# Kernel optimization log

Hardware: AMD Instinct MI355X
Metric: run time of the kernel (lower is better)

The kernel has to match this reference:

```python
import jax, jax.numpy as jnp
import numpy as np

MAX_SPAN_LEN = 6

def setup_inputs() -> dict:
    key = jax.random.key(0)
    k1, k2 = jax.random.split(key)
    B, L, H = 16, 1024, 768
    span_adjacency = jax.random.uniform(k1, (B, L, L, 1), dtype=jnp.float32)
    bound_hidden = jax.random.normal(k2, (B, L, H), dtype=jnp.float32)
    return {"span_adjacency": span_adjacency, "bound_hidden": bound_hidden}

def reference(span_adjacency, bound_hidden):
    # out[:, j] = sum_{i=j}^{min(j+6,L)-1} w[:,j,i] * concat(h[:,i], h[:,j])
    B, L, H = bound_hidden.shape
    d = jnp.arange(MAX_SPAN_LEN)                      # window offsets [6]
    j = jnp.arange(L)                                  # [L]
    idx = jnp.minimum(j[:, None] + d[None, :], L - 1)  # [L, 6] clamped gather index
    valid = (j[:, None] + d[None, :]) < L              # [L, 6] window mask
    # gather window weights: w[:, j, j+d] -> [B, L, 6]
    w = span_adjacency[:, j[:, None], idx, 0] * valid.astype(span_adjacency.dtype)
    # gather window hiddens: h[:, j+d] -> [B, L, 6, H]
    h_win = bound_hidden[:, idx]
    first = jnp.einsum('bjd,bjdh->bjh', w, h_win)      # sum_i w * h_i
    wsum = jnp.sum(w, axis=-1, keepdims=True)          # [B, L, 1]
    second = bound_hidden * wsum                       # h_j * sum_i w
    return jnp.concatenate([first, second], axis=-1)   # [B, L, 2H]
```

## Files before the change

### kernel.cpp

```cpp
#include <hip/hip_runtime.h>
#include <hip/hip_bf16.h>


#define LROWS 1024
#define HDIM  768
#define SPANW 6
#define TILE_J 8
#define STAGE (TILE_J + SPANW - 1)
#define VEC_PER_ROW (HDIM / 4)
#define WPT (TILE_J * VEC_PER_ROW / 256)

typedef float f32x4 __attribute__((ext_vector_type(4)));

__global__ __launch_bounds__(256) void boundary_seg_kernel(
    const float* __restrict__ span,
    const float* __restrict__ bound,
    float* __restrict__ out)
{
    __shared__ float sb[STAGE * HDIM];
    __shared__ float sw[TILE_J][SPANW];
    __shared__ float swsum[TILE_J];

    const int tid = threadIdx.x;
    const int b   = blockIdx.x >> 7;
    const int j0  = (blockIdx.x & 127) * TILE_J;
    const int bL  = b * LROWS;

    f32x4* sb4 = (f32x4*)sb;
    for (int i = tid; i < STAGE * VEC_PER_ROW; i += 256) {
        const int s  = i / VEC_PER_ROW;
        const int hv = i % VEC_PER_ROW;
        int gr = j0 + s;
        if (gr > LROWS - 1) gr = LROWS - 1;
        sb4[i] = *(const f32x4*)(bound + (size_t)(bL + gr) * HDIM + hv * 4);
    }

    if (tid < TILE_J) {
        const int j = j0 + tid;
        const float* srow = span + (size_t)(bL + j) * LROWS + j;
        float wsum = 0.f;
#pragma unroll
        for (int d = 0; d < SPANW; ++d) {
            float wd = (j + d < LROWS) ? srow[d] : 0.f;
            sw[tid][d] = wd;
            wsum += wd;
        }
        swsum[tid] = wsum;
    }
    __syncthreads();

#pragma unroll
    for (int k = 0; k < WPT; ++k) {
        const int item = tid + k * 256;
        const int jj   = item / VEC_PER_ROW;
        const int hv   = item % VEC_PER_ROW;

        f32x4 acc = (f32x4)(0.f);
        f32x4 h0;
#pragma unroll
        for (int d = 0; d < SPANW; ++d) {
            const float wd = sw[jj][d];
            const f32x4 h = sb4[(jj + d) * VEC_PER_ROW + hv];
            if (d == 0) h0 = h;
            acc += wd * h;
        }
        const f32x4 sec = h0 * swsum[jj];

        float* orow = out + (size_t)(bL + j0 + jj) * (2 * HDIM) + hv * 4;
        __builtin_nontemporal_store(acc, (f32x4*)orow);
        __builtin_nontemporal_store(sec, (f32x4*)(orow + HDIM));
    }
}

extern "C" void kernel_launch(void* const* d_in, const int* in_sizes, int n_in,
                              void* d_out, int out_size, void* d_ws, size_t ws_size,
                              hipStream_t stream) {
    const float* span  = (const float*)d_in[0];
    const float* bound = (const float*)d_in[1];
    float* out = (float*)d_out;

    const int B = in_sizes[1] / (LROWS * HDIM);
    dim3 grid(B * (LROWS / TILE_J)), block(256);
    hipLaunchKernelGGL(boundary_seg_kernel, grid, block, 0, stream,
                       span, bound, out);
}
```

Baseline: 182.0 us.

## Double-buffer bound rows via global_load_lds across multiple tiles per block

```diff
diff --git a/kernel.cpp b/kernel.cpp
--- a/kernel.cpp
+++ b/kernel.cpp
@@ -1,74 +1,102 @@
 #include <hip/hip_runtime.h>
-#include <hip/hip_bf16.h>
 
 
 #define LROWS 1024
 #define HDIM  768
 #define SPANW 6
 #define TILE_J 8
-#define STAGE (TILE_J + SPANW - 1)
-#define VEC_PER_ROW (HDIM / 4)
-#define WPT (TILE_J * VEC_PER_ROW / 256)
+#define STAGE 13
+#define VPR   (HDIM / 4)
+#define NT    4
+#define BLK   192
 
 typedef float f32x4 __attribute__((ext_vector_type(4)));
 
-__global__ __launch_bounds__(256) void boundary_seg_kernel(
+__device__ __forceinline__ void gload16(const float* g, float* l) {
+    __builtin_amdgcn_global_load_lds(
+        (const __attribute__((address_space(1))) void*)g,
+        (__attribute__((address_space(3))) void*)l,
+        16, 0, 0);
+}
+
+__global__ __launch_bounds__(BLK) void boundary_seg_kernel(
     const float* __restrict__ span,
     const float* __restrict__ bound,
     float* __restrict__ out)
 {
-    __shared__ float sb[STAGE * HDIM];
-    __shared__ float sw[TILE_J][SPANW];
-    __shared__ float swsum[TILE_J];
+    __shared__ __align__(16) float sb[2][STAGE * HDIM];
+    __shared__ __align__(16) float sw[2][TILE_J][8];
 
-    const int tid = threadIdx.x;
-    const int b   = blockIdx.x >> 7;
-    const int j0  = (blockIdx.x & 127) * TILE_J;
-    const int bL  = b * LROWS;
+    const int tid   = threadIdx.x;
+    const int b     = blockIdx.x >> 5;
+    const int strip = (blockIdx.x & 31) * (NT * TILE_J);
+    const int bL    = b * LROWS;
 
-    f32x4* sb4 = (f32x4*)sb;
-    for (int i = tid; i < STAGE * VEC_PER_ROW; i += 256) {
-        const int s  = i / VEC_PER_ROW;
-        const int hv = i % VEC_PER_ROW;
-        int gr = j0 + s;
-        if (gr > LROWS - 1) gr = LROWS - 1;
-        sb4[i] = *(const f32x4*)(bound + (size_t)(bL + gr) * HDIM + hv * 4);
-    }
+    const int sr = tid >> 3;
+    const int sd = tid & 7;
 
-    if (tid < TILE_J) {
-        const int j = j0 + tid;
-        const float* srow = span + (size_t)(bL + j) * LROWS + j;
-        float wsum = 0.f;
+    {
+        const int jt0 = strip;
 #pragma unroll
-        for (int d = 0; d < SPANW; ++d) {
-            float wd = (j + d < LROWS) ? srow[d] : 0.f;
-            sw[tid][d] = wd;
-            wsum += wd;
+        for (int r = 0; r < STAGE; ++r) {
+            int gr = jt0 + r; if (gr > LROWS - 1) gr = LROWS - 1;
+            gload16(bound + (size_t)(bL + gr) * HDIM + (tid << 2),
+                    &sb[0][r * HDIM + (tid << 2)]);
         }
-        swsum[tid] = wsum;
+        if (tid < 64) {
+            const int j = jt0 + sr;
+            float wd = 0.f;
+            if (sd < SPANW && j + sd < LROWS)
+                wd = span[(size_t)(bL + j) * LROWS + j + sd];
+            sw[0][sr][sd] = wd;
+        }
     }
     __syncthreads();
 
 #pragma unroll
-    for (int k = 0; k < WPT; ++k) {
-        const int item = tid + k * 256;
-        const int jj   = item / VEC_PER_ROW;
-        const int hv   = item % VEC_PER_ROW;
+    for (int t = 0; t < NT; ++t) {
+        const int cur = t & 1, nxt = cur ^ 1;
+        const int jt0 = strip + t * TILE_J;
 
-        f32x4 acc = (f32x4)(0.f);
-        f32x4 h0;
+        float wreg = 0.f;
+        if (t < NT - 1) {
+            const int jn = jt0 + TILE_J;
 #pragma unroll
-        for (int d = 0; d < SPANW; ++d) {
-            const float wd = sw[jj][d];
-            const f32x4 h = sb4[(jj + d) * VEC_PER_ROW + hv];
-            if (d == 0) h0 = h;
-            acc += wd * h;
+            for (int r = 0; r < STAGE; ++r) {
+                int gr = jn + r; if (gr > LROWS - 1) gr = LROWS - 1;
+                gload16(bound + (size_t)(bL + gr) * HDIM + (tid << 2),
+                        &sb[nxt][r * HDIM + (tid << 2)]);
+            }
+            if (tid < 64) {
+                const int j = jn + sr;
+                if (sd < SPANW && j + sd < LROWS)
+                    wreg = span[(size_t)(bL + j) * LROWS + j + sd];
+            }
         }
-        const f32x4 sec = h0 * swsum[jj];
+        __builtin_amdgcn_sched_barrier(0);
 
-        float* orow = out + (size_t)(bL + j0 + jj) * (2 * HDIM) + hv * 4;
-        __builtin_nontemporal_store(acc, (f32x4*)orow);
-        __builtin_nontemporal_store(sec, (f32x4*)(orow + HDIM));
+        const f32x4* sb4 = (const f32x4*)&sb[cur][0];
+        f32x4 h[STAGE];
+#pragma unroll
+        for (int r = 0; r < STAGE; ++r) h[r] = sb4[r * VPR + tid];
+
+#pragma unroll
+        for (int jj = 0; jj < TILE_J; ++jj) {
+            const f32x4 w0 = *(const f32x4*)&sw[cur][jj][0];
+            const f32x4 w1 = *(const f32x4*)&sw[cur][jj][4];
+            f32x4 acc = w0[0] * h[jj]     + w0[1] * h[jj + 1]
+                      + w0[2] * h[jj + 2] + w0[3] * h[jj + 3]
+                      + w1[0] * h[jj + 4] + w1[1] * h[jj + 5];
+            const float wsum = w0[0] + w0[1] + w0[2] + w0[3] + w1[0] + w1[1];
+            const f32x4 sec = h[jj] * wsum;
+
+            float* orow = out + (size_t)(bL + jt0 + jj) * (2 * HDIM) + (tid << 2);
+            *(f32x4*)orow          = acc;
+            *(f32x4*)(orow + HDIM) = sec;
+        }
+
+        if (t < NT - 1 && tid < 64) sw[nxt][sr][sd] = wreg;
+        __syncthreads();
     }
 }
 
@@ -80,7 +108,7 @@
     float* out = (float*)d_out;
 
     const int B = in_sizes[1] / (LROWS * HDIM);
-    dim3 grid(B * (LROWS / TILE_J)), block(256);
+    dim3 grid(B * (LROWS / (NT * TILE_J))), block(BLK);
     hipLaunchKernelGGL(boundary_seg_kernel, grid, block, 0, stream,
                        span, bound, out);
 }
```

Result: no change. 179.5 us (-1.4%).

## Replace LDS staging with per-thread register sliding window over row chunks

Applied to the files above, without the earlier changes.

```diff
diff --git a/kernel.cpp b/kernel.cpp
--- a/kernel.cpp
+++ b/kernel.cpp
@@ -1,74 +1,57 @@
 #include <hip/hip_runtime.h>
-#include <hip/hip_bf16.h>
 
 
 #define LROWS 1024
 #define HDIM  768
 #define SPANW 6
-#define TILE_J 8
-#define STAGE (TILE_J + SPANW - 1)
-#define VEC_PER_ROW (HDIM / 4)
-#define WPT (TILE_J * VEC_PER_ROW / 256)
+#define HALO  (SPANW - 1)
+#define RCHUNK 16
+#define CHUNKS (LROWS / RCHUNK)
+#define BLK   384
 
-typedef float f32x4 __attribute__((ext_vector_type(4)));
+typedef float f32x2 __attribute__((ext_vector_type(2)));
 
-__global__ __launch_bounds__(256) void boundary_seg_kernel(
+__global__ __launch_bounds__(BLK) void boundary_seg_kernel(
     const float* __restrict__ span,
     const float* __restrict__ bound,
     float* __restrict__ out)
 {
-    __shared__ float sb[STAGE * HDIM];
-    __shared__ float sw[TILE_J][SPANW];
-    __shared__ float swsum[TILE_J];
+    const int tid  = threadIdx.x;
+    const int b    = blockIdx.x >> 6;
+    const int j0   = (blockIdx.x & (CHUNKS - 1)) * RCHUNK;
+    const int bL   = b * LROWS;
+    const int colf = tid << 1;
 
-    const int tid = threadIdx.x;
-    const int b   = blockIdx.x >> 7;
-    const int j0  = (blockIdx.x & 127) * TILE_J;
-    const int bL  = b * LROWS;
-
-    f32x4* sb4 = (f32x4*)sb;
-    for (int i = tid; i < STAGE * VEC_PER_ROW; i += 256) {
-        const int s  = i / VEC_PER_ROW;
-        const int hv = i % VEC_PER_ROW;
-        int gr = j0 + s;
+    const float* bcol = bound + (size_t)bL * HDIM + colf;
+    f32x2 h[RCHUNK + HALO];
+#pragma unroll
+    for (int r = 0; r < RCHUNK + HALO; ++r) {
+        int gr = j0 + r;
         if (gr > LROWS - 1) gr = LROWS - 1;
-        sb4[i] = *(const f32x4*)(bound + (size_t)(bL + gr) * HDIM + hv * 4);
+        h[r] = *(const f32x2*)(bcol + (size_t)gr * HDIM);
     }
 
-    if (tid < TILE_J) {
-        const int j = j0 + tid;
-        const float* srow = span + (size_t)(bL + j) * LROWS + j;
-        float wsum = 0.f;
+    const float* sdiag = span + (size_t)(bL + j0) * LROWS + j0;
+
+#pragma unroll
+    for (int s = 0; s < RCHUNK; ++s) {
+        const int j = j0 + s;
+        const float* sp = sdiag + (size_t)s * (LROWS + 1);
+
+        float w[SPANW], wsum = 0.f;
 #pragma unroll
         for (int d = 0; d < SPANW; ++d) {
-            float wd = (j + d < LROWS) ? srow[d] : 0.f;
-            sw[tid][d] = wd;
-            wsum += wd;
+            w[d] = (j + d < LROWS) ? sp[d] : 0.f;
+            wsum += w[d];
         }
-        swsum[tid] = wsum;
-    }
-    __syncthreads();
 
-#pragma unroll
-    for (int k = 0; k < WPT; ++k) {
-        const int item = tid + k * 256;
-        const int jj   = item / VEC_PER_ROW;
-        const int hv   = item % VEC_PER_ROW;
+        f32x2 acc = w[0] * h[s]     + w[1] * h[s + 1] + w[2] * h[s + 2]
+                  + w[3] * h[s + 3] + w[4] * h[s + 4] + w[5] * h[s + 5];
+        const f32x2 sec = h[s] * wsum;
 
-        f32x4 acc = (f32x4)(0.f);
-        f32x4 h0;
-#pragma unroll
-        for (int d = 0; d < SPANW; ++d) {
-            const float wd = sw[jj][d];
-            const f32x4 h = sb4[(jj + d) * VEC_PER_ROW + hv];
-            if (d == 0) h0 = h;
-            acc += wd * h;
-        }
-        const f32x4 sec = h0 * swsum[jj];
-
-        float* orow = out + (size_t)(bL + j0 + jj) * (2 * HDIM) + hv * 4;
-        __builtin_nontemporal_store(acc, (f32x4*)orow);
-        __builtin_nontemporal_store(sec, (f32x4*)(orow + HDIM));
+        float* orow = out + (size_t)(bL + j) * (2 * HDIM) + colf;
+        *(f32x2*)orow          = acc;
+        *(f32x2*)(orow + HDIM) = sec;
     }
 }
 
@@ -80,7 +63,7 @@
     float* out = (float*)d_out;
 
     const int B = in_sizes[1] / (LROWS * HDIM);
-    dim3 grid(B * (LROWS / TILE_J)), block(256);
+    dim3 grid(B * CHUNKS), block(BLK);
     hipLaunchKernelGGL(boundary_seg_kernel, grid, block, 0, stream,
                        span, bound, out);
 }
```

Measured after the change: 180.9 us. No clear change (-0.6%).
